# Kernel optimization log

Measured on AMD Instinct MI355X. Metric: run time of the kernel, lower is better.

The kernel has to match this reference:

```python
import jax, jax.numpy as jnp
import numpy as np

NUM_NODE = 100000
DEG = 16
E = NUM_NODE * DEG
IN_C = 128
HID_C = 128
NUM_REL = 8


def setup_inputs() -> dict:
    key = jax.random.key(0)
    k1, k2, k3, k4, k5, k6 = jax.random.split(key, 6)
    x = jax.random.normal(k1, (NUM_NODE, IN_C), dtype=jnp.float32)
    # glorot-style init for relation weights [num_rel, in, hid]
    scale = jnp.sqrt(6.0 / (IN_C + HID_C)).astype(jnp.float32)
    rel_weight = jax.random.uniform(k2, (NUM_REL, IN_C, HID_C), dtype=jnp.float32, minval=-1.0, maxval=1.0) * scale
    # uniform-degree CSR so every node has deg >= 1 (avoids div-by-zero, matches module assumption)
    ptr = jnp.arange(NUM_NODE + 1, dtype=jnp.int64) * DEG
    idx = jax.random.randint(k3, (E,), 0, NUM_NODE, dtype=jnp.int64)
    edge_types = jax.random.randint(k4, (E,), 0, NUM_REL, dtype=jnp.int64)
    # about 1/3 of nodes have cached history (value != -1)
    history_map = jax.random.randint(k5, (NUM_NODE,), -1, 2, dtype=jnp.int64)
    history_buffer = jax.random.normal(k6, (NUM_NODE, HID_C), dtype=jnp.float32)
    return {
        'x': x,
        'rel_weight': rel_weight,
        'ptr': ptr,
        'idx': idx,
        'edge_types': edge_types,
        'history_map': history_map,
        'history_buffer': history_buffer,
        'history_size': 1,
        'num_node': NUM_NODE,
    }


def reference(x, rel_weight, ptr, idx, edge_types, history_map, history_buffer, history_size, num_node):
    E_ = idx.shape[0]
    num_rel = rel_weight.shape[0]
    hid = rel_weight.shape[2]
    xg = x[idx]                                   # [E, in] gather of source features
    # relation-grouped transform: small static loop over relations, masked accumulate
    msgs = jnp.zeros((E_, hid), dtype=x.dtype)
    for r in range(num_rel):
        msgs = msgs + jnp.where((edge_types == r)[:, None], xg @ rel_weight[r], jnp.zeros((), x.dtype))
    deg = ptr[1:] - ptr[:-1]                      # [num_node]
    seg = jnp.repeat(jnp.arange(num_node), deg, total_repeat_length=E_)  # dst id per edge
    out = jax.ops.segment_sum(msgs, seg, num_segments=num_node)          # scatter-sum
    out = out / deg[:, None].astype(out.dtype)    # degree normalization
    if history_size > 0:                          # static python int
        out = jnp.where((history_map != -1)[:, None], history_buffer, out)
    return (out, out)
```

## Files before the change

kernel.cpp:

```cpp
#include <hip/hip_runtime.h>
#include <stdint.h>

#define IN_C   128
#define HID_C  128
#define NREL   8
#define K_TOTAL (NREL * IN_C)
#define TILE_M  16
#define SRB     1032

typedef float  f32x4  __attribute__((ext_vector_type(4)));
typedef __bf16 bf16x8 __attribute__((ext_vector_type(8)));
typedef short  s16x8  __attribute__((ext_vector_type(8)));
typedef unsigned short u16;

__device__ __forceinline__ unsigned short f2bf(float f) {
    unsigned int u = __float_as_uint(f);
    u += 0x7fffu + ((u >> 16) & 1u);
    return (unsigned short)(u >> 16);
}

__global__ void zero_count_kernel(unsigned int* count) { *count = 0u; }

__global__ __launch_bounds__(256) void prep_kernel(
        const float* __restrict__ W,
        const int* __restrict__ hmap, const float* __restrict__ hbuf,
        unsigned short* __restrict__ Wt,
        int* __restrict__ list, unsigned int* __restrict__ count,
        float* __restrict__ out, int NN, int WE) {
    int gid = blockIdx.x * blockDim.x + threadIdx.x;

    {
        bool active = (gid < NN) && (hmap[gid] == -1);
        unsigned long long mask = __ballot(active);
        if (mask) {
            int lane   = threadIdx.x & 63;
            int leader = __ffsll((unsigned long long)mask) - 1;
            unsigned base = 0;
            if (lane == leader) base = atomicAdd(count, (unsigned)__popcll(mask));
            base = __shfl(base, leader, 64);
            if (active) {
                int off = __popcll(mask & ((1ull << lane) - 1ull));
                list[base + off] = gid;
            }
        }
    }

    int n = gid >> 5;
    int q = gid & 31;
    if (n < NN) {
        if (hmap[n] != -1) {
            f32x4 v = ((const f32x4*)hbuf)[(size_t)n * 32 + q];
            f32x4* o = (f32x4*)out;
            o[(size_t)n * 32 + q] = v;
            o[(size_t)NN * 32 + (size_t)n * 32 + q] = v;
        }
    }

    if (gid < WE) {
        int r   = gid >> 14;
        int rem = gid & 16383;
        int k   = rem >> 7;
        int c   = rem & 127;
        Wt[(size_t)c * K_TOTAL + r * IN_C + k] = f2bf(W[gid]);
    }
}

__global__ __launch_bounds__(256, 4) void gemm_kernel(
        const float* __restrict__ x,
        const int* __restrict__ ptr,
        const int* __restrict__ idx,
        const int* __restrict__ ety,
        const unsigned short* __restrict__ Wt,
        const int* __restrict__ list,
        const unsigned int* __restrict__ count,
        float* __restrict__ out, int NN) {
    __shared__ u16      S[TILE_M * SRB];
    __shared__ unsigned meta[TILE_M * 16];
    __shared__ int      nids[TILE_M];
    __shared__ int      degs[TILE_M];
    __shared__ float    invdeg[TILE_M];

    unsigned int cnt = *count;
    int rowbase = blockIdx.x * TILE_M;
    if (rowbase >= (int)cnt) return;

    int t = threadIdx.x;
    if (t < TILE_M) {
        int row = rowbase + t;
        int nid = -1, d = 0; float idg = 0.f;
        if (row < (int)cnt) {
            nid = list[row];
            int e0 = ptr[nid], e1 = ptr[nid + 1];
            d = e1 - e0;
            idg = (d > 0) ? 1.0f / (float)d : 0.f;
        }
        nids[t] = nid; degs[t] = d; invdeg[t] = idg;
    }
    __syncthreads();

    int n = t >> 4;
    int c = t & 15;
    int nid = nids[n];
    int deg = degs[n];
    int e0  = (nid >= 0) ? ptr[nid] : 0;

    int maxdeg = 0;
    #pragma unroll
    for (int i = 0; i < TILE_M; ++i) maxdeg = max(maxdeg, degs[i]);

    f32x4 alo[NREL], ahi[NREL];
    #pragma unroll
    for (int r = 0; r < NREL; ++r) { alo[r] = f32x4{0,0,0,0}; ahi[r] = f32x4{0,0,0,0}; }

    const float* xc = x + c * 8;

    for (int jb = 0; jb < maxdeg; jb += 16) {
        {
            int j = jb + c;
            unsigned m = 0xFFFFFFFFu;
            if (nid >= 0 && j < deg) {
                int e = e0 + j;
                m = ((unsigned)idx[e]) | (((unsigned)ety[e]) << 27);
            }
            meta[t] = m;
        }
        __syncthreads();

        unsigned mm[16];
        {
            uint4 q0 = *(const uint4*)(meta + (n << 4) + 0);
            uint4 q1 = *(const uint4*)(meta + (n << 4) + 4);
            uint4 q2 = *(const uint4*)(meta + (n << 4) + 8);
            uint4 q3 = *(const uint4*)(meta + (n << 4) + 12);
            mm[0]=q0.x;  mm[1]=q0.y;  mm[2]=q0.z;  mm[3]=q0.w;
            mm[4]=q1.x;  mm[5]=q1.y;  mm[6]=q1.z;  mm[7]=q1.w;
            mm[8]=q2.x;  mm[9]=q2.y;  mm[10]=q2.z; mm[11]=q2.w;
            mm[12]=q3.x; mm[13]=q3.y; mm[14]=q3.z; mm[15]=q3.w;
        }
        int offs[16];
        int rel[16];
        #pragma unroll
        for (int j = 0; j < 16; ++j) {
            unsigned m = mm[j];
            bool valid = (m != 0xFFFFFFFFu);
            int src = valid ? (int)(m & 0x07FFFFFFu) : 0;
            rel[j]  = valid ? (int)(m >> 27) : 31;
            offs[j] = src * IN_C;
        }

        f32x4 blo[4], bhi[4];
        #pragma unroll
        for (int u = 0; u < 4; ++u) {
            const f32x4* p = (const f32x4*)(xc + offs[u]);
            blo[u] = p[0]; bhi[u] = p[1];
        }
        #pragma unroll
        for (int b = 0; b < 4; ++b) {
            f32x4 nlo[4], nhi[4];
            if (b < 3) {
                #pragma unroll
                for (int u = 0; u < 4; ++u) {
                    const f32x4* p = (const f32x4*)(xc + offs[(b + 1) * 4 + u]);
                    nlo[u] = p[0]; nhi[u] = p[1];
                }
            }
            #pragma unroll
            for (int u = 0; u < 4; ++u) {
                int r = rel[b * 4 + u];
                #pragma unroll
                for (int rr = 0; rr < NREL; ++rr) {
                    float mk = (r == rr) ? 1.0f : 0.0f;
                    alo[rr] += blo[u] * mk;
                    ahi[rr] += bhi[u] * mk;
                }
            }
            if (b < 3) {
                #pragma unroll
                for (int u = 0; u < 4; ++u) { blo[u] = nlo[u]; bhi[u] = nhi[u]; }
            }
        }
        __syncthreads();
    }

    {
        u16* srow = S + n * SRB + c * 8;
        #pragma unroll
        for (int rr = 0; rr < NREL; ++rr) {
            s16x8 pk;
            pk[0] = (short)f2bf(alo[rr][0]); pk[1] = (short)f2bf(alo[rr][1]);
            pk[2] = (short)f2bf(alo[rr][2]); pk[3] = (short)f2bf(alo[rr][3]);
            pk[4] = (short)f2bf(ahi[rr][0]); pk[5] = (short)f2bf(ahi[rr][1]);
            pk[6] = (short)f2bf(ahi[rr][2]); pk[7] = (short)f2bf(ahi[rr][3]);
            *(s16x8*)(srow + rr * IN_C) = pk;
        }
    }
    __syncthreads();

    int wave = t >> 6, lane = t & 63;
    int quad = lane >> 4, l16 = lane & 15;
    int chbase = wave * 32;
    const u16* arow  = S + l16 * SRB + quad * 8;
    const u16* bbase = Wt + (size_t)(chbase + l16) * K_TOTAL + quad * 8;

    f32x4 acc0 = {0.f,0.f,0.f,0.f};
    f32x4 acc1 = {0.f,0.f,0.f,0.f};
    #pragma unroll 8
    for (int ks = 0; ks < K_TOTAL; ks += 32) {
        s16x8 a  = *(const s16x8*)(arow + ks);
        s16x8 b0 = *(const s16x8*)(bbase + ks);
        s16x8 b1 = *(const s16x8*)(bbase + ks + 16 * K_TOTAL);
        union { s16x8 s; bf16x8 b; } ua, ub0, ub1;
        ua.s = a; ub0.s = b0; ub1.s = b1;
        acc0 = __builtin_amdgcn_mfma_f32_16x16x32_bf16(ua.b, ub0.b, acc0, 0, 0, 0);
        acc1 = __builtin_amdgcn_mfma_f32_16x16x32_bf16(ua.b, ub1.b, acc1, 0, 0, 0);
    }

    size_t half = (size_t)NN * HID_C;
    #pragma unroll
    for (int v = 0; v < 4; ++v) {
        int rowl = quad * 4 + v;
        int onid = nids[rowl];
        if (onid < 0) continue;
        float s = invdeg[rowl];
        float v0 = acc0[v] * s;
        float v1 = acc1[v] * s;
        size_t o0 = (size_t)onid * HID_C + chbase + l16;
        out[o0]             = v0;
        out[o0 + 16]        = v1;
        out[o0 + half]      = v0;
        out[o0 + 16 + half] = v1;
    }
}

extern "C" void kernel_launch(void* const* d_in, const int* in_sizes, int n_in,
                              void* d_out, int out_size, void* d_ws, size_t ws_size,
                              hipStream_t stream) {
    const float* x    = (const float*)d_in[0];
    const float* W    = (const float*)d_in[1];
    const int*   ptr  = (const int*)d_in[2];
    const int*   idx  = (const int*)d_in[3];
    const int*   ety  = (const int*)d_in[4];
    const int*   hmap = (const int*)d_in[5];
    const float* hbuf = (const float*)d_in[6];
    int NN = in_sizes[5];
    int WE = in_sizes[1];
    float* out = (float*)d_out;

    unsigned int* count = (unsigned int*)d_ws;
    int* list = (int*)((char*)d_ws + 256);
    size_t wt_off = 256 + (((size_t)NN * 4 + 4095) / 4096) * 4096;
    unsigned short* Wt = (unsigned short*)((char*)d_ws + wt_off);

    zero_count_kernel<<<1, 1, 0, stream>>>(count);

    long long tot = (long long)NN * 32;
    if (tot < (long long)WE) tot = WE;
    prep_kernel<<<(int)((tot + 255) / 256), 256, 0, stream>>>(
        W, hmap, hbuf, Wt, list, count, out, NN, WE);

    gemm_kernel<<<(NN + TILE_M - 1) / TILE_M, 256, 0, stream>>>(
        x, ptr, idx, ety, Wt, list, count, out, NN);
}
```

Measured before the change: 303.0 us.

## Precompute compacted per-node edge metadata in prep kernel, broadcast via shuffles

The prep kernel now writes, for each non-cached node, a packed (node, e0, degree) record and its first 16 edges' packed source/relation words into a contiguous compacted array. The gemm kernel reads these with one coalesced load per thread and distributes them with wave shuffles, which removes the dependent ptr→idx/ety chain and the LDS meta round-trip plus barrier from the first 16 edges. Nodes with more than 16 edges fall back to the old LDS path. The cost is that prep threads now do serial scattered loads of 16 edges each, and the fast path is only a full fit for degree ≤ 16.

```diff
diff --git a/kernel.cpp b/kernel.cpp
--- a/kernel.cpp
+++ b/kernel.cpp
@@ -10,7 +10,7 @@
 
 typedef float  f32x4  __attribute__((ext_vector_type(4)));
 typedef __bf16 bf16x8 __attribute__((ext_vector_type(8)));
-typedef short  s16x8  __attribute__((ext_vector_type(8)));
+typedef short  s16x8 __attribute__((ext_vector_type(8)));
 typedef unsigned short u16;
 
 __device__ __forceinline__ unsigned short f2bf(float f) {
@@ -24,8 +24,11 @@
 __global__ __launch_bounds__(256) void prep_kernel(
         const float* __restrict__ W,
         const int* __restrict__ hmap, const float* __restrict__ hbuf,
+        const int* __restrict__ ptr, const int* __restrict__ idx,
+        const int* __restrict__ ety,
         unsigned short* __restrict__ Wt,
-        int* __restrict__ list, unsigned int* __restrict__ count,
+        int4* __restrict__ list2, unsigned* __restrict__ emeta,
+        unsigned int* __restrict__ count,
         float* __restrict__ out, int NN, int WE) {
     int gid = blockIdx.x * blockDim.x + threadIdx.x;
 
@@ -40,7 +43,19 @@
             base = __shfl(base, leader, 64);
             if (active) {
                 int off = __popcll(mask & ((1ull << lane) - 1ull));
-                list[base + off] = gid;
+                int p   = (int)base + off;
+                int e0  = ptr[gid], e1 = ptr[gid + 1];
+                int d   = e1 - e0;
+                list2[p] = int4{gid, e0, d, 0};
+                #pragma unroll
+                for (int j = 0; j < 16; ++j) {
+                    unsigned m = 0xFFFFFFFFu;
+                    if (j < d) {
+                        int e = e0 + j;
+                        m = ((unsigned)idx[e]) | (((unsigned)ety[e]) << 27);
+                    }
+                    emeta[(size_t)p * 16 + j] = m;
+                }
             }
         }
     }
@@ -67,46 +82,57 @@
 
 __global__ __launch_bounds__(256, 4) void gemm_kernel(
         const float* __restrict__ x,
-        const int* __restrict__ ptr,
         const int* __restrict__ idx,
         const int* __restrict__ ety,
         const unsigned short* __restrict__ Wt,
-        const int* __restrict__ list,
+        const int4* __restrict__ list2,
+        const unsigned* __restrict__ emeta,
         const unsigned int* __restrict__ count,
         float* __restrict__ out, int NN) {
     __shared__ u16      S[TILE_M * SRB];
-    __shared__ unsigned meta[TILE_M * 16];
     __shared__ int      nids[TILE_M];
+    __shared__ int      e0s[TILE_M];
     __shared__ int      degs[TILE_M];
     __shared__ float    invdeg[TILE_M];
+    __shared__ unsigned meta_x[256];
 
     unsigned int cnt = *count;
     int rowbase = blockIdx.x * TILE_M;
     if (rowbase >= (int)cnt) return;
 
     int t = threadIdx.x;
-    if (t < TILE_M) {
-        int row = rowbase + t;
-        int nid = -1, d = 0; float idg = 0.f;
-        if (row < (int)cnt) {
-            nid = list[row];
-            int e0 = ptr[nid], e1 = ptr[nid + 1];
-            d = e1 - e0;
-            idg = (d > 0) ? 1.0f / (float)d : 0.f;
-        }
-        nids[t] = nid; degs[t] = d; invdeg[t] = idg;
-    }
-    __syncthreads();
-
     int n = t >> 4;
     int c = t & 15;
-    int nid = nids[n];
-    int deg = degs[n];
-    int e0  = (nid >= 0) ? ptr[nid] : 0;
-
-    int maxdeg = 0;
-    #pragma unroll
-    for (int i = 0; i < TILE_M; ++i) maxdeg = max(maxdeg, degs[i]);
+    int lane = t & 63;
+
+    bool vrow = (rowbase + n) < (int)cnt;
+    unsigned mymeta = vrow ? emeta[(size_t)rowbase * 16 + t] : 0xFFFFFFFFu;
+
+    if (t < TILE_M) {
+        int nid = -1, e0 = 0, d = 0; float idg = 0.f;
+        if (rowbase + t < (int)cnt) {
+            int4 L = list2[rowbase + t];
+            nid = L.x; e0 = L.y; d = L.z;
+            idg = (d > 0) ? 1.0f / (float)d : 0.f;
+        }
+        nids[t] = nid; e0s[t] = e0; degs[t] = d; invdeg[t] = idg;
+    }
+
+    unsigned mm[16];
+    #pragma unroll
+    for (int j = 0; j < 16; ++j)
+        mm[j] = __shfl(mymeta, (lane & 48) | j, 64);
+
+    int offs[16];
+    int rel[16];
+    #pragma unroll
+    for (int j = 0; j < 16; ++j) {
+        unsigned m = mm[j];
+        bool valid = (m != 0xFFFFFFFFu);
+        int src = valid ? (int)(m & 0x07FFFFFFu) : 0;
+        rel[j]  = valid ? (int)(m >> 27) : 31;
+        offs[j] = src * IN_C;
+    }
 
     f32x4 alo[NREL], ahi[NREL];
     #pragma unroll
@@ -114,40 +140,7 @@
 
     const float* xc = x + c * 8;
 
-    for (int jb = 0; jb < maxdeg; jb += 16) {
-        {
-            int j = jb + c;
-            unsigned m = 0xFFFFFFFFu;
-            if (nid >= 0 && j < deg) {
-                int e = e0 + j;
-                m = ((unsigned)idx[e]) | (((unsigned)ety[e]) << 27);
-            }
-            meta[t] = m;
-        }
-        __syncthreads();
-
-        unsigned mm[16];
-        {
-            uint4 q0 = *(const uint4*)(meta + (n << 4) + 0);
-            uint4 q1 = *(const uint4*)(meta + (n << 4) + 4);
-            uint4 q2 = *(const uint4*)(meta + (n << 4) + 8);
-            uint4 q3 = *(const uint4*)(meta + (n << 4) + 12);
-            mm[0]=q0.x;  mm[1]=q0.y;  mm[2]=q0.z;  mm[3]=q0.w;
-            mm[4]=q1.x;  mm[5]=q1.y;  mm[6]=q1.z;  mm[7]=q1.w;
-            mm[8]=q2.x;  mm[9]=q2.y;  mm[10]=q2.z; mm[11]=q2.w;
-            mm[12]=q3.x; mm[13]=q3.y; mm[14]=q3.z; mm[15]=q3.w;
-        }
-        int offs[16];
-        int rel[16];
-        #pragma unroll
-        for (int j = 0; j < 16; ++j) {
-            unsigned m = mm[j];
-            bool valid = (m != 0xFFFFFFFFu);
-            int src = valid ? (int)(m & 0x07FFFFFFu) : 0;
-            rel[j]  = valid ? (int)(m >> 27) : 31;
-            offs[j] = src * IN_C;
-        }
-
+    {
         f32x4 blo[4], bhi[4];
         #pragma unroll
         for (int u = 0; u < 4; ++u) {
@@ -179,7 +172,48 @@
                 for (int u = 0; u < 4; ++u) { blo[u] = nlo[u]; bhi[u] = nhi[u]; }
             }
         }
-        __syncthreads();
+    }
+    __syncthreads();
+
+    int md = 0;
+    #pragma unroll
+    for (int i = 0; i < TILE_M; ++i) md = max(md, degs[i]);
+    if (md > TILE_M) {
+        int nid_n = nids[n], deg_n = degs[n], e0_n = e0s[n];
+        for (int jb = TILE_M; jb < md; jb += TILE_M) {
+            {
+                int j = jb + c;
+                unsigned m = 0xFFFFFFFFu;
+                if (nid_n >= 0 && j < deg_n) {
+                    int e = e0_n + j;
+                    m = ((unsigned)idx[e]) | (((unsigned)ety[e]) << 27);
+                }
+                meta_x[t] = m;
+            }
+            __syncthreads();
+            uint4 q0 = *(const uint4*)(meta_x + (n << 4) + 0);
+            uint4 q1 = *(const uint4*)(meta_x + (n << 4) + 4);
+            uint4 q2 = *(const uint4*)(meta_x + (n << 4) + 8);
+            uint4 q3 = *(const uint4*)(meta_x + (n << 4) + 12);
+            unsigned mx[16] = {q0.x,q0.y,q0.z,q0.w, q1.x,q1.y,q1.z,q1.w,
+                               q2.x,q2.y,q2.z,q2.w, q3.x,q3.y,q3.z,q3.w};
+            #pragma unroll
+            for (int j = 0; j < 16; ++j) {
+                unsigned m = mx[j];
+                bool valid = (m != 0xFFFFFFFFu);
+                int src = valid ? (int)(m & 0x07FFFFFFu) : 0;
+                int r   = valid ? (int)(m >> 27) : 31;
+                const f32x4* p = (const f32x4*)(xc + src * IN_C);
+                f32x4 lo = p[0], hi = p[1];
+                #pragma unroll
+                for (int rr = 0; rr < NREL; ++rr) {
+                    float mk = (r == rr) ? 1.0f : 0.0f;
+                    alo[rr] += lo * mk;
+                    ahi[rr] += hi * mk;
+                }
+            }
+            __syncthreads();
+        }
     }
 
     {
@@ -196,7 +230,7 @@
     }
     __syncthreads();
 
-    int wave = t >> 6, lane = t & 63;
+    int wave = t >> 6;
     int quad = lane >> 4, l16 = lane & 15;
     int chbase = wave * 32;
     const u16* arow  = S + l16 * SRB + quad * 8;
@@ -247,17 +281,19 @@
     float* out = (float*)d_out;
 
     unsigned int* count = (unsigned int*)d_ws;
-    int* list = (int*)((char*)d_ws + 256);
-    size_t wt_off = 256 + (((size_t)NN * 4 + 4095) / 4096) * 4096;
+    int4* list2 = (int4*)((char*)d_ws + 256);
+    size_t wt_off = 256 + (((size_t)NN * 16 + 4095) / 4096) * 4096;
     unsigned short* Wt = (unsigned short*)((char*)d_ws + wt_off);
+    size_t em_off = ((wt_off + (size_t)K_TOTAL * HID_C * 2 + 4095) / 4096) * 4096;
+    unsigned* emeta = (unsigned*)((char*)d_ws + em_off);
 
     zero_count_kernel<<<1, 1, 0, stream>>>(count);
 
     long long tot = (long long)NN * 32;
     if (tot < (long long)WE) tot = WE;
     prep_kernel<<<(int)((tot + 255) / 256), 256, 0, stream>>>(
-        W, hmap, hbuf, Wt, list, count, out, NN, WE);
+        W, hmap, hbuf, ptr, idx, ety, Wt, list2, emeta, count, out, NN, WE);
 
     gemm_kernel<<<(NN + TILE_M - 1) / TILE_M, 256, 0, stream>>>(
-        x, ptr, idx, ety, Wt, list, count, out, NN);
-}
+        x, idx, ety, Wt, list2, emeta, count, out, NN);
+}
```

Result: no change. 302.8 us (-0.1%).
